# Kernel tuning notes

Measured on AMD Instinct MI355X. Metric: run time of the kernel, lower is better.

## Reference

```python
import jax, jax.numpy as jnp
import numpy as np

S, B, D, H = 2048, 2, 1024, 16
DK = D // H


def rotate_half(x):
    # interleaved variant: pairs (x0,x1)->(-x1,x0)
    x1 = x[..., ::2]
    x2 = x[..., 1::2]
    return jnp.stack((-x2, x1), axis=-1).reshape(x.shape)


def apply_rope(x):
    # x: [B, H, S, dk]
    b, h, s, dk = x.shape
    pos = jnp.arange(s, dtype=jnp.float32)
    inv_freq = 1.0 / (10000.0 ** (jnp.arange(0, dk, 2, dtype=jnp.float32) / dk))
    freqs = jnp.einsum('i,j->ij', pos, inv_freq)          # [S, dk/2]
    emb = jnp.concatenate((freqs, freqs), axis=-1)        # [S, dk]  (non-interleaved cos/sin, as in source)
    cos = jnp.cos(emb)[None, None, :, :]
    sin = jnp.sin(emb)[None, None, :, :]
    return x * cos + rotate_half(x) * sin


def setup_inputs() -> dict:
    key = jax.random.key(0)
    ks = jax.random.split(key, 11)
    sc = 0.02
    return {
        'query': jax.random.normal(ks[0], (S, B, D), jnp.float32),
        'key':   jax.random.normal(ks[1], (S, B, D), jnp.float32),
        'value': jax.random.normal(ks[2], (S, B, D), jnp.float32),
        'wq': jax.random.normal(ks[3], (D, D), jnp.float32) * sc,
        'bq': jax.random.normal(ks[4], (D,), jnp.float32) * sc,
        'wk': jax.random.normal(ks[5], (D, D), jnp.float32) * sc,
        'bk': jax.random.normal(ks[6], (D,), jnp.float32) * sc,
        'wv': jax.random.normal(ks[7], (D, D), jnp.float32) * sc,
        'bv': jax.random.normal(ks[8], (D,), jnp.float32) * sc,
        'wo': jax.random.normal(ks[9], (D, D), jnp.float32) * sc,
        'bo': jax.random.normal(ks[10], (D,), jnp.float32) * sc,
    }


def reference(query, key, value, wq, bq, wk, bk, wv, bv, wo, bo):
    s_q, b, _ = query.shape
    s_k = key.shape[0]

    def split_heads(x, s):
        # [S,B,D] -> [B,H,S,dk]
        return x.transpose(1, 0, 2).reshape(b, s, H, DK).transpose(0, 2, 1, 3)

    Q = split_heads(query @ wq.T + bq, s_q)
    K = split_heads(key @ wk.T + bk, s_k)
    V = split_heads(value @ wv.T + bv, s_k)

    Q = apply_rope(Q)
    K = apply_rope(K)

    scores = jnp.einsum('bhqd,bhkd->bhqk', Q, K) / jnp.sqrt(jnp.float32(DK))
    attn = jax.nn.softmax(scores, axis=-1)
    out = jnp.einsum('bhqk,bhkd->bhqd', attn, V)          # [B,H,Sq,dk]
    out = out.transpose(0, 2, 1, 3).reshape(b, s_q, D)    # [B,Sq,D]
    out = out.transpose(1, 0, 2)                          # [Sq,B,D]
    return out @ wo.T + bo
```

## Files before the change

### kernel.cpp

```cpp
#include <hip/hip_runtime.h>
#include <cstdint>
#include <cstddef>

typedef __attribute__((ext_vector_type(4))) float f32x4;
typedef __attribute__((ext_vector_type(8))) float f32x8;
typedef __attribute__((ext_vector_type(16))) float f32x16;
typedef __attribute__((ext_vector_type(8))) __bf16 bf16x8;
typedef __attribute__((ext_vector_type(4))) __bf16 bf16x4;
typedef __attribute__((ext_vector_type(2))) __bf16 bf16x2;
typedef __attribute__((ext_vector_type(4))) unsigned int u32x4;
typedef unsigned short u16;

#define S_LEN 2048
#define BATCH 2
#define DMODEL 1024
#define NHEAD 16
#define HDK 64

__device__ __forceinline__ u16 f2bf(float f) {
    uint32_t u = __float_as_uint(f);
    u += 0x7FFFu + ((u >> 16) & 1u);
    return (u16)(u >> 16);
}

__device__ __forceinline__ void gload_lds16(const void* g, void* l) {
    __builtin_amdgcn_global_load_lds(
        (const __attribute__((address_space(1))) uint32_t*)g,
        (__attribute__((address_space(3))) uint32_t*)l, 16, 0, 0);
}

__device__ __forceinline__ unsigned pk2(float a, float b) {
    bf16x2 t;
    t[0] = (__bf16)a; t[1] = (__bf16)b;
    return __builtin_bit_cast(unsigned, t);
}

__device__ __forceinline__ f32x16 z16() {
    f32x16 v = {0.f,0.f,0.f,0.f,0.f,0.f,0.f,0.f,0.f,0.f,0.f,0.f,0.f,0.f,0.f,0.f};
    return v;
}

__global__ __launch_bounds__(256) void cvt_kernel(
    const float* __restrict__ a0, const float* __restrict__ a1, const float* __restrict__ a2,
    const float* __restrict__ a3, const float* __restrict__ a4, const float* __restrict__ a5,
    const float* __restrict__ a6,
    u16* __restrict__ o0, u16* __restrict__ o1, u16* __restrict__ o2,
    u16* __restrict__ o3, u16* __restrict__ o4, u16* __restrict__ o5,
    u16* __restrict__ o6)
{
    const int by = blockIdx.y;
    const float* s;
    u16* d;
    int n;
    switch (by) {
        case 0: s = a0; d = o0; n = 4194304; break;
        case 1: s = a1; d = o1; n = 4194304; break;
        case 2: s = a2; d = o2; n = 4194304; break;
        case 3: s = a3; d = o3; n = 1048576; break;
        case 4: s = a4; d = o4; n = 1048576; break;
        case 5: s = a5; d = o5; n = 1048576; break;
        default: s = a6; d = o6; n = 1048576; break;
    }
    int idx = (blockIdx.x * 256 + threadIdx.x) * 8;
    if (idx >= n) return;
    float4 f0 = *(const float4*)(s + idx);
    float4 f1 = *(const float4*)(s + idx + 4);
    alignas(16) u16 o[8] = {f2bf(f0.x), f2bf(f0.y), f2bf(f0.z), f2bf(f0.w),
                            f2bf(f1.x), f2bf(f1.y), f2bf(f1.z), f2bf(f1.w)};
    *(u32x4*)(d + idx) = *(const u32x4*)o;
}

__global__ __launch_bounds__(512, 6) void qkv_kernel(
    const u16* __restrict__ X0, const u16* __restrict__ X1, const u16* __restrict__ X2,
    const u16* __restrict__ W0, const u16* __restrict__ W1, const u16* __restrict__ W2,
    const float* __restrict__ B0, const float* __restrict__ B1, const float* __restrict__ B2,
    u16* __restrict__ O0, u16* __restrict__ O1, u16* __restrict__ Vt)
{
    __shared__ __align__(16) u16 lA[2][128 * 32];
    __shared__ __align__(16) u16 lB[2][128 * 32];
    const int tid = threadIdx.x, wid = tid >> 6, lane = tid & 63;
    const int l15 = lane & 15, l4 = lane >> 4;
    const int p = blockIdx.y * 32 + blockIdx.x;
    const int vid = (p & 7) * 96 + (p >> 3);
    const int bx = vid & 31, byv = vid >> 5;
    const int mat = byv >> 3;
    const u16* X = mat == 0 ? X0 : (mat == 1 ? X1 : X2);
    const u16* W = mat == 0 ? W0 : (mat == 1 ? W1 : W2);
    const float* bias = mat == 0 ? B0 : (mat == 1 ? B1 : B2);
    const int m0 = bx * 128, n0 = (byv & 7) * 128;
    const int mw = (wid >> 1) * 32, nw = (wid & 1) * 64;

    f32x4 acc[2][4];
#pragma unroll
    for (int i = 0; i < 2; ++i)
#pragma unroll
        for (int j = 0; j < 4; ++j) acc[i][j] = (f32x4){0.f, 0.f, 0.f, 0.f};

    const int srow = tid >> 2, sg = (tid & 3) ^ (srow & 3);

#define QSTAGE(bufi, k0_) do {                                                \
        gload_lds16(X + (size_t)(m0 + srow) * 1024 + (k0_) + sg * 8,          \
                    (char*)lA + (bufi) * 8192 + (tid & ~63) * 16);            \
        gload_lds16(W + (size_t)(n0 + srow) * 1024 + (k0_) + sg * 8,          \
                    (char*)lB + (bufi) * 8192 + (tid & ~63) * 16);            \
    } while (0)

    QSTAGE(0, 0);
    for (int ks = 0; ks < 32; ++ks) {
        const int cur = ks & 1;
        if (ks < 31) {
            QSTAGE(cur ^ 1, (ks + 1) * 32);
            asm volatile("s_waitcnt vmcnt(2)" ::: "memory");
        } else {
            asm volatile("s_waitcnt vmcnt(0)" ::: "memory");
        }
        __builtin_amdgcn_s_barrier();
        const char* la = (const char*)lA + cur * 8192;
        const char* lb = (const char*)lB + cur * 8192;
        __builtin_amdgcn_s_setprio(1);
        bf16x8 af[2], bfr[4];
#pragma unroll
        for (int f = 0; f < 2; ++f) {
            int ra = mw + f * 16 + l15;
            af[f] = *(const bf16x8*)(la + ra * 64 +
                    ((l4 * 16) ^ ((ra & 3) << 4)));
        }
#pragma unroll
        for (int f = 0; f < 4; ++f) {
            int rb = nw + f * 16 + l15;
            bfr[f] = *(const bf16x8*)(lb + rb * 64 +
                    ((l4 * 16) ^ ((rb & 3) << 4)));
        }
#pragma unroll
        for (int mf = 0; mf < 2; ++mf)
#pragma unroll
            for (int nf = 0; nf < 4; ++nf)
                acc[mf][nf] = __builtin_amdgcn_mfma_f32_16x16x32_bf16(
                    af[mf], bfr[nf], acc[mf][nf], 0, 0, 0);
        __builtin_amdgcn_s_setprio(0);
        __builtin_amdgcn_s_barrier();
    }
#undef QSTAGE

    if (mat < 2) {
        u16* O = mat == 0 ? O0 : O1;
#pragma unroll
        for (int mf = 0; mf < 2; ++mf) {
#pragma unroll
            for (int nf = 0; nf < 4; ++nf) {
                int gcol = n0 + nw + nf * 16 + l15;
                float bval = bias[gcol];
                int h = gcol >> 6, d = gcol & 63;
                float invf = __expf(-(float)(d & 31) * 0.2878231366f);
#pragma unroll
                for (int i = 0; i < 4; ++i) {
                    int grow = m0 + mw + mf * 16 + l4 * 4 + i;
                    int s = grow >> 1, b = grow & 1;
                    float v = acc[mf][nf][i] + bval;
                    float p2 = __shfl_xor(v, 1);
                    float th = (float)s * invf;
                    float sn, cs;
                    __sincosf(th, &sn, &cs);
                    v = (d & 1) ? fmaf(p2, sn, v * cs) : fmaf(-p2, sn, v * cs);
                    if (mat == 0) v *= 0.18033688f;
                    O[((size_t)(b * NHEAD + h) * S_LEN + s) * HDK + d] = f2bf(v);
                }
            }
        }
    } else {
        u16 vout[2][4][4];
#pragma unroll
        for (int mf = 0; mf < 2; ++mf)
#pragma unroll
            for (int nf = 0; nf < 4; ++nf) {
                float bval = bias[n0 + nw + nf * 16 + l15];
#pragma unroll
                for (int i = 0; i < 4; ++i)
                    vout[mf][nf][i] = f2bf(acc[mf][nf][i] + bval);
            }
        u16* t = (u16*)lA;
        const int half = wid & 1;
        const int rd = tid >> 3, rjc = tid & 7;
#pragma unroll
        for (int h_ = 0; h_ < 2; ++h_) {
            const int hh = (n0 >> 6) + h_;
#pragma unroll
            for (int bb = 0; bb < 2; ++bb) {
                __syncthreads();
                if (half == h_) {
#pragma unroll
                    for (int mf = 0; mf < 2; ++mf)
#pragma unroll
                        for (int nf = 0; nf < 4; ++nf)
#pragma unroll
                            for (int i2 = 0; i2 < 2; ++i2) {
                                int i = bb + i2 * 2;
                                int rowL = mw + mf * 16 + l4 * 4 + i;
                                t[(rowL >> 1) * 72 + nf * 16 + l15] = vout[mf][nf][i];
                            }
                }
                __syncthreads();
                alignas(16) u16 tmp[8];
#pragma unroll
                for (int x = 0; x < 8; ++x) {
                    int lp = (rjc & 1) * 8 + x;
                    int sl = (lp & 3) | ((lp & 4) << 1) | ((lp & 8) >> 1);
                    tmp[x] = t[((rjc >> 1) * 16 + sl) * 72 + rd];
                }
                *(bf16x8*)(void*)(Vt + ((size_t)(bb * NHEAD + hh) * HDK + rd) * S_LEN
                                  + (m0 >> 1) + rjc * 8) = *(const bf16x8*)tmp;
            }
        }
    }
}

__global__ __launch_bounds__(512, 4) void attn_kernel(
    const u16* __restrict__ Q, const u16* __restrict__ K,
    const u16* __restrict__ V, u16* __restrict__ O)
{
    __shared__ __align__(16) char smem[65536];
    const int tid = threadIdx.x, wid = tid >> 6, lane = tid & 63;
    const int g = wid >> 2, wv = wid & 3;
    const int l31 = lane & 31, hi = lane >> 5;
    const int p = blockIdx.y * 16 + blockIdx.x;
    const int vid = (p & 7) * 64 + (p >> 3);
    const int bh = vid >> 4, b = bh >> 4, h = bh & 15;
    const int q0 = (vid & 15) * 128;
    const u16* Qb = Q + (size_t)bh * S_LEN * HDK;
    const u16* Kb = K + (size_t)bh * S_LEN * HDK;
    const u16* Vb = V + (size_t)bh * HDK * S_LEN;

    const int qrow = q0 + wv * 32 + l31;
    bf16x8 aq[4];
#pragma unroll
    for (int ks = 0; ks < 4; ++ks)
        aq[ks] = *(const bf16x8*)(const void*)(Qb + (size_t)qrow * HDK + ks * 16 + hi * 8);

    f32x16 acc0 = z16(), acc1 = z16();
    float lpart = 0.f;

    char* gbase = smem + g * 32768;
    const int gt = tid & 255;
    const int srow = gt >> 3, lg = (gt & 7) ^ (srow & 7);
    char* sK = gbase + wv * 1024;
    char* sV = gbase + 8192 + wv * 1024;
    const u16* pk0 = Kb + (size_t)(g * 1024 + srow) * HDK + lg * 8;
    const u16* pk1 = pk0 + 32 * HDK;
    const u16* pv0 = Vb + (size_t)srow * S_LEN + g * 1024 + lg * 8;
    const u16* pv1 = pv0 + (size_t)32 * S_LEN;

    const int swl = (l31 & 7) << 4;
    const char* akr[4];
    const char* avr[4];
#pragma unroll
    for (int i = 0; i < 4; ++i) {
        akr[i] = gbase + l31 * 128 + ((i * 32 + hi * 16) ^ swl);
        avr[i] = gbase + 8192 + l31 * 128 + ((i * 32 + hi * 16) ^ swl);
    }

    gload_lds16(pk0, sK);
    gload_lds16(pk1, sK + 4096);
    gload_lds16(pv0, sV);
    gload_lds16(pv1, sV + 4096);
    pk0 += 4096; pk1 += 4096; pv0 += 64; pv1 += 64;

#define TILE(CUR_, STG_) do {                                                 \
    if (STG_) {                                                               \
        gload_lds16(pk0, sK + ((CUR_) ^ 1) * 16384);                          \
        gload_lds16(pk1, sK + ((CUR_) ^ 1) * 16384 + 4096);                   \
        gload_lds16(pv0, sV + ((CUR_) ^ 1) * 16384);                          \
        gload_lds16(pv1, sV + ((CUR_) ^ 1) * 16384 + 4096);                   \
        pk0 += 4096; pk1 += 4096; pv0 += 64; pv1 += 64;                       \
        asm volatile("s_waitcnt vmcnt(4)" ::: "memory");                      \
    } else {                                                                  \
        asm volatile("s_waitcnt vmcnt(0)" ::: "memory");                      \
    }                                                                         \
    __builtin_amdgcn_s_barrier();                                             \
    f32x16 s0 = z16(), s1 = z16();                                            \
    __builtin_amdgcn_s_setprio(1);                                            \
    _Pragma("unroll")                                                         \
    for (int ks = 0; ks < 4; ++ks) {                                          \
        bf16x8 a0 = *(const bf16x8*)(akr[ks] + (CUR_) * 16384);               \
        s0 = __builtin_amdgcn_mfma_f32_32x32x16_bf16(a0, aq[ks], s0, 0, 0, 0);\
    }                                                                         \
    _Pragma("unroll")                                                         \
    for (int ks = 0; ks < 4; ++ks) {                                          \
        bf16x8 a1 = *(const bf16x8*)(akr[ks] + (CUR_) * 16384 + 4096);        \
        s1 = __builtin_amdgcn_mfma_f32_32x32x16_bf16(a1, aq[ks], s1, 0, 0, 0);\
    }                                                                         \
    __builtin_amdgcn_s_setprio(0);                                            \
    _Pragma("unroll")                                                         \
    for (int i = 0; i < 16; ++i) {                                            \
        s0[i] = __builtin_amdgcn_exp2f(s0[i]);                                \
        s1[i] = __builtin_amdgcn_exp2f(s1[i]);                                \
    }                                                                         \
    {                                                                         \
        f32x16 sm_ = s0 + s1;                                                 \
        f32x8 q8_ = __builtin_shufflevector(sm_, sm_, 0,1,2,3,4,5,6,7)        \
                  + __builtin_shufflevector(sm_, sm_, 8,9,10,11,12,13,14,15); \
        f32x4 q4_ = __builtin_shufflevector(q8_, q8_, 0,1,2,3)                \
                  + __builtin_shufflevector(q8_, q8_, 4,5,6,7);               \
        lpart += (q4_[0] + q4_[1]) + (q4_[2] + q4_[3]);                       \
    }                                                                         \
    __builtin_amdgcn_s_setprio(1);                                            \
    _Pragma("unroll")                                                         \
    for (int i = 0; i < 4; ++i) {                                             \
        const f32x16* cp = (i >> 1) ? &s1 : &s0;                              \
        const int e0 = (i & 1) * 8;                                           \
        u32x4 bw;                                                             \
        bw[0] = pk2((*cp)[e0 + 0], (*cp)[e0 + 1]);                            \
        bw[1] = pk2((*cp)[e0 + 2], (*cp)[e0 + 3]);                            \
        bw[2] = pk2((*cp)[e0 + 4], (*cp)[e0 + 5]);                            \
        bw[3] = pk2((*cp)[e0 + 6], (*cp)[e0 + 7]);                            \
        bf16x8 Bf = __builtin_bit_cast(bf16x8, bw);                           \
        bf16x8 av0 = *(const bf16x8*)(avr[i] + (CUR_) * 16384);               \
        bf16x8 av1 = *(const bf16x8*)(avr[i] + (CUR_) * 16384 + 4096);        \
        acc0 = __builtin_amdgcn_mfma_f32_32x32x16_bf16(av0, Bf, acc0, 0, 0, 0);\
        acc1 = __builtin_amdgcn_mfma_f32_32x32x16_bf16(av1, Bf, acc1, 0, 0, 0);\
    }                                                                         \
    __builtin_amdgcn_s_setprio(0);                                            \
    __builtin_amdgcn_s_barrier();                                             \
} while (0)

    for (int th = 0; th < 8; ++th) {
        TILE(0, 1);
        TILE(1, (th < 7));
    }
#undef TILE

    lpart += __shfl_xor(lpart, 32);
    float* exO = (float*)smem;
    float* exL = (float*)(smem + 36864);
    const int sl = wv * 64 + lane;
    if (g == 1) {
#pragma unroll
        for (int r4 = 0; r4 < 4; ++r4) {
            f32x4 w0 = {acc0[r4 * 4 + 0], acc0[r4 * 4 + 1], acc0[r4 * 4 + 2], acc0[r4 * 4 + 3]};
            f32x4 w1 = {acc1[r4 * 4 + 0], acc1[r4 * 4 + 1], acc1[r4 * 4 + 2], acc1[r4 * 4 + 3]};
            *(f32x4*)(exO + sl * 36 + r4 * 4) = w0;
            *(f32x4*)(exO + sl * 36 + 16 + r4 * 4) = w1;
        }
        exL[sl] = lpart;
    }
    __syncthreads();
    if (g == 0) {
        float l1 = exL[sl];
        float rl = 1.0f / (lpart + l1);
        u16* obase = O + ((size_t)qrow * BATCH + b) * DMODEL + h * HDK;
#pragma unroll
        for (int db = 0; db < 2; ++db) {
#pragma unroll
            for (int r4 = 0; r4 < 4; ++r4) {
                f32x4 part = *(const f32x4*)(exO + sl * 36 + db * 16 + r4 * 4);
                bf16x4 outv;
#pragma unroll
                for (int e = 0; e < 4; ++e) {
                    float own = db ? acc1[r4 * 4 + e] : acc0[r4 * 4 + e];
                    outv[e] = (__bf16)((own + part[e]) * rl);
                }
                *(bf16x4*)(void*)(obase + db * 32 + 8 * r4 + 4 * hi) = outv;
            }
        }
    }
}

__global__ __launch_bounds__(256) void proj_kernel(
    const u16* __restrict__ A, const u16* __restrict__ W,
    const float* __restrict__ bias, float* __restrict__ out)
{
    __shared__ __align__(16) u16 lA[2][64 * 64];
    __shared__ __align__(16) u16 lB[2][128 * 64];
    const int tid = threadIdx.x, wid = tid >> 6, lane = tid & 63;
    const int l15 = lane & 15, l4 = lane >> 4;
    const int p = blockIdx.y * 8 + blockIdx.x;
    const int vid = (p & 7) * 64 + (p >> 3);
    const int m0 = (vid & 63) * 64, n0 = (vid >> 6) * 128;
    const int nw = wid * 32;

    f32x4 acc[4][2];
#pragma unroll
    for (int i = 0; i < 4; ++i)
#pragma unroll
        for (int j = 0; j < 2; ++j) acc[i][j] = (f32x4){0.f, 0.f, 0.f, 0.f};

#define PSTAGE(bufi, k0_) do {                                                \
        _Pragma("unroll")                                                     \
        for (int it = 0; it < 2; ++it) {                                      \
            int cc = it * 256 + tid;                                          \
            int row = cc >> 3, gg = (cc & 7) ^ (row & 7);                     \
            gload_lds16(A + (size_t)(m0 + row) * 1024 + (k0_) + gg * 8,       \
                        (char*)lA + (bufi) * 8192 + (cc & ~63) * 16);         \
        }                                                                     \
        _Pragma("unroll")                                                     \
        for (int it = 0; it < 4; ++it) {                                      \
            int cc = it * 256 + tid;                                          \
            int row = cc >> 3, gg = (cc & 7) ^ (row & 7);                     \
            gload_lds16(W + (size_t)(n0 + row) * 1024 + (k0_) + gg * 8,       \
                        (char*)lB + (bufi) * 16384 + (cc & ~63) * 16);        \
        }                                                                     \
    } while (0)

    PSTAGE(0, 0);
    for (int ks = 0; ks < 16; ++ks) {
        const int cur = ks & 1;
        if (ks < 15) {
            PSTAGE(cur ^ 1, (ks + 1) * 64);
            asm volatile("s_waitcnt vmcnt(6)" ::: "memory");
        } else {
            asm volatile("s_waitcnt vmcnt(0)" ::: "memory");
        }
        __builtin_amdgcn_s_barrier();
        const char* la = (const char*)lA + cur * 8192;
        const char* lb = (const char*)lB + cur * 16384;
        __builtin_amdgcn_s_setprio(1);
#pragma unroll
        for (int kk = 0; kk < 2; ++kk) {
            bf16x8 af[4], bfr[2];
#pragma unroll
            for (int f = 0; f < 4; ++f) {
                int ra = f * 16 + l15;
                af[f] = *(const bf16x8*)(la + ra * 128 +
                        ((kk * 64 + l4 * 16) ^ ((ra & 7) << 4)));
            }
#pragma unroll
            for (int f = 0; f < 2; ++f) {
                int rb = nw + f * 16 + l15;
                bfr[f] = *(const bf16x8*)(lb + rb * 128 +
                        ((kk * 64 + l4 * 16) ^ ((rb & 7) << 4)));
            }
#pragma unroll
            for (int mf = 0; mf < 4; ++mf)
#pragma unroll
                for (int nf = 0; nf < 2; ++nf)
                    acc[mf][nf] = __builtin_amdgcn_mfma_f32_16x16x32_bf16(
                        af[mf], bfr[nf], acc[mf][nf], 0, 0, 0);
        }
        __builtin_amdgcn_s_setprio(0);
        __builtin_amdgcn_s_barrier();
    }
#undef PSTAGE

#pragma unroll
    for (int mf = 0; mf < 4; ++mf) {
#pragma unroll
        for (int nf = 0; nf < 2; ++nf) {
            int gcol = n0 + nw + nf * 16 + l15;
            float bval = bias[gcol];
#pragma unroll
            for (int i = 0; i < 4; ++i) {
                int grow = m0 + mf * 16 + l4 * 4 + i;
                out[(size_t)grow * DMODEL + gcol] = acc[mf][nf][i] + bval;
            }
        }
    }
}

extern "C" void kernel_launch(void* const* d_in, const int* in_sizes, int n_in,
                              void* d_out, int out_size, void* d_ws, size_t ws_size,
                              hipStream_t stream)
{
    (void)in_sizes; (void)n_in; (void)out_size; (void)ws_size;
    const float* q  = (const float*)d_in[0];
    const float* k  = (const float*)d_in[1];
    const float* v  = (const float*)d_in[2];
    const float* wq = (const float*)d_in[3];
    const float* bq = (const float*)d_in[4];
    const float* wk = (const float*)d_in[5];
    const float* bk = (const float*)d_in[6];
    const float* wv = (const float*)d_in[7];
    const float* bv = (const float*)d_in[8];
    const float* wo = (const float*)d_in[9];
    const float* bo = (const float*)d_in[10];

    char* ws = (char*)d_ws;
    const size_t MB = 1024 * 1024;
    u16* XQ  = (u16*)(ws + 0 * MB);
    u16* XK  = (u16*)(ws + 8 * MB);
    u16* XV  = (u16*)(ws + 16 * MB);
    u16* WQb = (u16*)(ws + 24 * MB);
    u16* WKb = (u16*)(ws + 26 * MB);
    u16* WVb = (u16*)(ws + 28 * MB);
    u16* WOb = (u16*)(ws + 30 * MB);
    u16* QR  = (u16*)(ws + 32 * MB);
    u16* KR  = (u16*)(ws + 40 * MB);
    u16* VT  = (u16*)(ws + 48 * MB);
    u16* OA  = XQ;

    cvt_kernel<<<dim3(2048, 7), 256, 0, stream>>>(q, k, v, wq, wk, wv, wo,
                                                  XQ, XK, XV, WQb, WKb, WVb, WOb);
    qkv_kernel<<<dim3(32, 24), 512, 0, stream>>>(XQ, XK, XV, WQb, WKb, WVb,
                                                 bq, bk, bv, QR, KR, VT);
    attn_kernel<<<dim3(16, 32), 512, 0, stream>>>(QR, KR, VT, OA);
    proj_kernel<<<dim3(8, 64), 256, 0, stream>>>(OA, WOb, bo, (float*)d_out);
}
```

Measured before the change: 114.5 us.

## Fuse fp32-to-bf16 activation conversion into QKV GEMM A-operand staging

```diff
diff --git a/kernel.cpp b/kernel.cpp
--- a/kernel.cpp
+++ b/kernel.cpp
@@ -41,28 +41,15 @@
 }
 
 __global__ __launch_bounds__(256) void cvt_kernel(
-    const float* __restrict__ a0, const float* __restrict__ a1, const float* __restrict__ a2,
-    const float* __restrict__ a3, const float* __restrict__ a4, const float* __restrict__ a5,
-    const float* __restrict__ a6,
+    const float* __restrict__ a0, const float* __restrict__ a1,
+    const float* __restrict__ a2, const float* __restrict__ a3,
     u16* __restrict__ o0, u16* __restrict__ o1, u16* __restrict__ o2,
-    u16* __restrict__ o3, u16* __restrict__ o4, u16* __restrict__ o5,
-    u16* __restrict__ o6)
+    u16* __restrict__ o3)
 {
     const int by = blockIdx.y;
-    const float* s;
-    u16* d;
-    int n;
-    switch (by) {
-        case 0: s = a0; d = o0; n = 4194304; break;
-        case 1: s = a1; d = o1; n = 4194304; break;
-        case 2: s = a2; d = o2; n = 4194304; break;
-        case 3: s = a3; d = o3; n = 1048576; break;
-        case 4: s = a4; d = o4; n = 1048576; break;
-        case 5: s = a5; d = o5; n = 1048576; break;
-        default: s = a6; d = o6; n = 1048576; break;
-    }
+    const float* s = by == 0 ? a0 : (by == 1 ? a1 : (by == 2 ? a2 : a3));
+    u16* d = by == 0 ? o0 : (by == 1 ? o1 : (by == 2 ? o2 : o3));
     int idx = (blockIdx.x * 256 + threadIdx.x) * 8;
-    if (idx >= n) return;
     float4 f0 = *(const float4*)(s + idx);
     float4 f1 = *(const float4*)(s + idx + 4);
     alignas(16) u16 o[8] = {f2bf(f0.x), f2bf(f0.y), f2bf(f0.z), f2bf(f0.w),
@@ -71,7 +58,7 @@
 }
 
 __global__ __launch_bounds__(512, 6) void qkv_kernel(
-    const u16* __restrict__ X0, const u16* __restrict__ X1, const u16* __restrict__ X2,
+    const float* __restrict__ X0, const float* __restrict__ X1, const float* __restrict__ X2,
     const u16* __restrict__ W0, const u16* __restrict__ W1, const u16* __restrict__ W2,
     const float* __restrict__ B0, const float* __restrict__ B1, const float* __restrict__ B2,
     u16* __restrict__ O0, u16* __restrict__ O1, u16* __restrict__ Vt)
@@ -84,7 +71,7 @@
     const int vid = (p & 7) * 96 + (p >> 3);
     const int bx = vid & 31, byv = vid >> 5;
     const int mat = byv >> 3;
-    const u16* X = mat == 0 ? X0 : (mat == 1 ? X1 : X2);
+    const float* X = mat == 0 ? X0 : (mat == 1 ? X1 : X2);
     const u16* W = mat == 0 ? W0 : (mat == 1 ? W1 : W2);
     const float* bias = mat == 0 ? B0 : (mat == 1 ? B1 : B2);
     const int m0 = bx * 128, n0 = (byv & 7) * 128;
@@ -97,50 +84,77 @@
         for (int j = 0; j < 4; ++j) acc[i][j] = (f32x4){0.f, 0.f, 0.f, 0.f};
 
     const int srow = tid >> 2, sg = (tid & 3) ^ (srow & 3);
-
-#define QSTAGE(bufi, k0_) do {                                                \
-        gload_lds16(X + (size_t)(m0 + srow) * 1024 + (k0_) + sg * 8,          \
-                    (char*)lA + (bufi) * 8192 + (tid & ~63) * 16);            \
-        gload_lds16(W + (size_t)(n0 + srow) * 1024 + (k0_) + sg * 8,          \
-                    (char*)lB + (bufi) * 8192 + (tid & ~63) * 16);            \
+    const int arow = tid >> 2, alg = tid & 3;
+    const int awg = alg ^ (arow & 3);
+    u16* adst = (u16*)lA + arow * 32 + awg * 8;
+
+#define BISSUE(ks_, buf_) \
+    gload_lds16(W + (size_t)(n0 + srow) * 1024 + (ks_) * 32 + sg * 8, \
+                (char*)lB + (buf_) * 8192 + (tid & ~63) * 16)
+
+#define AISSUE(ks_, r0_, r1_) do { \
+        const float* asrc_ = X + (size_t)(m0 + arow) * 1024 + (ks_) * 32 + alg * 8; \
+        r0_ = *(const f32x4*)asrc_; \
+        r1_ = *(const f32x4*)(asrc_ + 4); \
     } while (0)
 
-    QSTAGE(0, 0);
-    for (int ks = 0; ks < 32; ++ks) {
-        const int cur = ks & 1;
-        if (ks < 31) {
-            QSTAGE(cur ^ 1, (ks + 1) * 32);
-            asm volatile("s_waitcnt vmcnt(2)" ::: "memory");
-        } else {
-            asm volatile("s_waitcnt vmcnt(0)" ::: "memory");
-        }
-        __builtin_amdgcn_s_barrier();
-        const char* la = (const char*)lA + cur * 8192;
-        const char* lb = (const char*)lB + cur * 8192;
-        __builtin_amdgcn_s_setprio(1);
-        bf16x8 af[2], bfr[4];
-#pragma unroll
-        for (int f = 0; f < 2; ++f) {
-            int ra = mw + f * 16 + l15;
-            af[f] = *(const bf16x8*)(la + ra * 64 +
-                    ((l4 * 16) ^ ((ra & 3) << 4)));
-        }
-#pragma unroll
-        for (int f = 0; f < 4; ++f) {
-            int rb = nw + f * 16 + l15;
-            bfr[f] = *(const bf16x8*)(lb + rb * 64 +
-                    ((l4 * 16) ^ ((rb & 3) << 4)));
-        }
-#pragma unroll
-        for (int mf = 0; mf < 2; ++mf)
-#pragma unroll
-            for (int nf = 0; nf < 4; ++nf)
-                acc[mf][nf] = __builtin_amdgcn_mfma_f32_16x16x32_bf16(
-                    af[mf], bfr[nf], acc[mf][nf], 0, 0, 0);
-        __builtin_amdgcn_s_setprio(0);
-        __builtin_amdgcn_s_barrier();
-    }
-#undef QSTAGE
+#define AWRITE(buf_, r0_, r1_) do { \
+        bf16x8 t_; \
+        t_[0] = (__bf16)r0_[0]; t_[1] = (__bf16)r0_[1]; \
+        t_[2] = (__bf16)r0_[2]; t_[3] = (__bf16)r0_[3]; \
+        t_[4] = (__bf16)r1_[0]; t_[5] = (__bf16)r1_[1]; \
+        t_[6] = (__bf16)r1_[2]; t_[7] = (__bf16)r1_[3]; \
+        *(bf16x8*)(void*)(adst + (buf_) * 4096) = t_; \
+    } while (0)
+
+    f32x4 a0r0, a0r1, a1r0, a1r1;
+    AISSUE(0, a0r0, a0r1); BISSUE(0, 0);
+    AISSUE(1, a1r0, a1r1); BISSUE(1, 1);
+    AWRITE(0, a0r0, a0r1);
+
+#define QSTEP(ks_, CUR, NXT, ARc0, ARc1, ARn0, ARn1, TOPVM, DOISS, DOWR) do { \
+        asm volatile("s_waitcnt vmcnt(" #TOPVM ") lgkmcnt(0)" ::: "memory");  \
+        __builtin_amdgcn_s_barrier();                                         \
+        {                                                                     \
+            const char* la = (const char*)lA + (CUR) * 8192;                  \
+            const char* lb = (const char*)lB + (CUR) * 8192;                  \
+            __builtin_amdgcn_s_setprio(1);                                    \
+            bf16x8 af[2], bfr[4];                                             \
+            _Pragma("unroll")                                                 \
+            for (int f = 0; f < 2; ++f) {                                     \
+                int ra = mw + f * 16 + l15;                                   \
+                af[f] = *(const bf16x8*)(la + ra * 64 +                       \
+                        ((l4 * 16) ^ ((ra & 3) << 4)));                       \
+            }                                                                 \
+            _Pragma("unroll")                                                 \
+            for (int f = 0; f < 4; ++f) {                                     \
+                int rb = nw + f * 16 + l15;                                   \
+                bfr[f] = *(const bf16x8*)(lb + rb * 64 +                      \
+                        ((l4 * 16) ^ ((rb & 3) << 4)));                       \
+            }                                                                 \
+            _Pragma("unroll")                                                 \
+            for (int mf = 0; mf < 2; ++mf)                                    \
+                _Pragma("unroll")                                             \
+                for (int nf = 0; nf < 4; ++nf)                                \
+                    acc[mf][nf] = __builtin_amdgcn_mfma_f32_16x16x32_bf16(    \
+                        af[mf], bfr[nf], acc[mf][nf], 0, 0, 0);               \
+            __builtin_amdgcn_s_setprio(0);                                    \
+        }                                                                     \
+        __builtin_amdgcn_s_barrier();                                         \
+        if (DOISS) { AISSUE((ks_) + 2, ARn0, ARn1); BISSUE((ks_) + 2, CUR); } \
+        if (DOWR)  { AWRITE(NXT, ARc0, ARc1); }                               \
+    } while (0)
+
+    for (int kh = 0; kh < 15; ++kh) {
+        QSTEP(2 * kh,     0, 1, a1r0, a1r1, a0r0, a0r1, 3, 1, 1);
+        QSTEP(2 * kh + 1, 1, 0, a0r0, a0r1, a1r0, a1r1, 3, (2 * kh + 1 <= 29), 1);
+    }
+    QSTEP(30, 0, 1, a1r0, a1r1, a0r0, a0r1, 3, 0, 1);
+    QSTEP(31, 1, 0, a0r0, a0r1, a1r0, a1r1, 0, 0, 0);
+#undef QSTEP
+#undef AWRITE
+#undef AISSUE
+#undef BISSUE
 
     if (mat < 2) {
         u16* O = mat == 0 ? O0 : O1;
@@ -474,9 +488,7 @@
 
     char* ws = (char*)d_ws;
     const size_t MB = 1024 * 1024;
-    u16* XQ  = (u16*)(ws + 0 * MB);
-    u16* XK  = (u16*)(ws + 8 * MB);
-    u16* XV  = (u16*)(ws + 16 * MB);
+    u16* OA  = (u16*)(ws + 0 * MB);
     u16* WQb = (u16*)(ws + 24 * MB);
     u16* WKb = (u16*)(ws + 26 * MB);
     u16* WVb = (u16*)(ws + 28 * MB);
@@ -484,11 +496,10 @@
     u16* QR  = (u16*)(ws + 32 * MB);
     u16* KR  = (u16*)(ws + 40 * MB);
     u16* VT  = (u16*)(ws + 48 * MB);
-    u16* OA  = XQ;
-
-    cvt_kernel<<<dim3(2048, 7), 256, 0, stream>>>(q, k, v, wq, wk, wv, wo,
-                                                  XQ, XK, XV, WQb, WKb, WVb, WOb);
-    qkv_kernel<<<dim3(32, 24), 512, 0, stream>>>(XQ, XK, XV, WQb, WKb, WVb,
+
+    cvt_kernel<<<dim3(512, 4), 256, 0, stream>>>(wq, wk, wv, wo,
+                                                 WQb, WKb, WVb, WOb);
+    qkv_kernel<<<dim3(32, 24), 512, 0, stream>>>(q, k, v, WQb, WKb, WVb,
                                                  bq, bk, bv, QR, KR, VT);
     attn_kernel<<<dim3(16, 32), 512, 0, stream>>>(QR, KR, VT, OA);
     proj_kernel<<<dim3(8, 64), 256, 0, stream>>>(OA, WOb, bo, (float*)d_out);
```

Result: no change. 115.6 us (+0.9%).
